# Optimization experiments

Measured on AMD Instinct MI355X. Metric: run time of the kernel, lower is better.

## Reference

```python
import jax, jax.numpy as jnp
import numpy as np

B, S, D, H = 2, 2048, 1024, 16
HD = D // H  # head dim = 64


def setup_inputs() -> dict:
    key = jax.random.key(0)
    ks = jax.random.split(key, 5)
    scale = 0.02
    x = jax.random.normal(ks[0], (B, S, D), dtype=jnp.float32)
    Wqkv = jax.random.normal(ks[1], (D, 3 * D), dtype=jnp.float32) * scale
    bqkv = jnp.zeros((3 * D,), dtype=jnp.float32)
    Wproj = jax.random.normal(ks[2], (D, D), dtype=jnp.float32) * scale
    bproj = jnp.zeros((D,), dtype=jnp.float32)
    return {"x": x, "Wqkv": Wqkv, "bqkv": bqkv, "Wproj": Wproj, "bproj": bproj}


def reference(x, Wqkv, bqkv, Wproj, bproj):
    # fused QKV projection
    qkv = x @ Wqkv + bqkv                      # [B, S, 3D]
    q, k, v = jnp.split(qkv, 3, axis=-1)       # each [B, S, D]
    # split heads -> [B, H, S, HD]
    def heads(t):
        return t.reshape(B, S, H, HD).transpose(0, 2, 1, 3)
    q, k, v = heads(q), heads(k), heads(v)
    # scaled dot-product attention with causal mask (GPT-2 style)
    scores = jnp.einsum('bhqd,bhkd->bhqk', q, k) / jnp.sqrt(jnp.float32(HD))
    causal = jnp.tril(jnp.ones((S, S), dtype=bool))
    scores = jnp.where(causal, scores, jnp.finfo(scores.dtype).min)
    attn = jax.nn.softmax(scores, axis=-1)      # [B, H, S, S]
    out = jnp.einsum('bhqk,bhkd->bhqd', attn, v)  # [B, H, S, HD]
    out = out.transpose(0, 2, 1, 3).reshape(B, S, D)
    return out @ Wproj + bproj
```

## Files before the change

### kernel.cpp

```cpp
#include <hip/hip_runtime.h>
#include <hip/hip_bf16.h>


typedef __attribute__((ext_vector_type(8))) short short8;
typedef __attribute__((ext_vector_type(4))) float float4v;

#define S_LEN 2048
#define NHEAD 16
#define HDIM  64
#define DMODEL 1024

__device__ __forceinline__ unsigned short f2bf(float f) {
    union { float f; unsigned u; } v; v.f = f;
    unsigned r = v.u + 0x7FFF + ((v.u >> 16) & 1);
    return (unsigned short)(r >> 16);
}

__device__ __forceinline__ unsigned fbits_rn(float f) {
    union { float f; unsigned u; } v; v.f = f;
    return v.u + 0x8000u;
}

__device__ __forceinline__ void async16(const void* g, const void* l) {
    __builtin_amdgcn_global_load_lds(
        (const __attribute__((address_space(1))) unsigned int*)g,
        (__attribute__((address_space(3))) unsigned int*)l, 16, 0, 0);
}

__global__ void f32_to_bf16_v4(const float4* __restrict__ in,
                               ushort4* __restrict__ out, int n4) {
    int i = blockIdx.x * blockDim.x + threadIdx.x;
    if (i < n4) {
        float4 v = in[i];
        ushort4 o;
        o.x = f2bf(v.x); o.y = f2bf(v.y); o.z = f2bf(v.z); o.w = f2bf(v.w);
        out[i] = o;
    }
}

__global__ __launch_bounds__(256) void w_transpose_bf16(
    const float* __restrict__ Wqkv, const float* __restrict__ Wproj,
    unsigned short* __restrict__ outQ, unsigned short* __restrict__ outP) {
    __shared__ float t[64][65];
    const float* in; unsigned short* out; int N, bxl;
    if (blockIdx.x < 48) { in = Wqkv;  out = outQ; N = 3072; bxl = blockIdx.x; }
    else                 { in = Wproj; out = outP; N = 1024; bxl = blockIdx.x - 48; }
    const int K = 1024;
    const int kb = blockIdx.y * 64, nb = bxl * 64;
    const int tid = threadIdx.x;
    const int r0 = tid >> 4, c0 = (tid & 15) * 4;
#pragma unroll
    for (int g = 0; g < 4; g++) {
        float4 v = *(const float4*)(in + (size_t)(kb + g * 16 + r0) * N + nb + c0);
        t[g * 16 + r0][c0 + 0] = v.x; t[g * 16 + r0][c0 + 1] = v.y;
        t[g * 16 + r0][c0 + 2] = v.z; t[g * 16 + r0][c0 + 3] = v.w;
    }
    __syncthreads();
#pragma unroll
    for (int g = 0; g < 4; g++) {
        int n = g * 16 + r0;
        ushort4 o;
        o.x = f2bf(t[c0 + 0][n]); o.y = f2bf(t[c0 + 1][n]);
        o.z = f2bf(t[c0 + 2][n]); o.w = f2bf(t[c0 + 3][n]);
        *(ushort4*)(out + (size_t)(nb + n) * K + kb + c0) = o;
    }
}

__global__ __launch_bounds__(256) void v_transpose_sw(
    const unsigned short* __restrict__ V, unsigned short* __restrict__ Vt) {
    __shared__ unsigned short t[64 * 68];
    const int bh = blockIdx.y;
    const int s0 = blockIdx.x * 64;
    const int tid = threadIdx.x;
    const int r = tid >> 2;
    const int c4 = tid & 3;
    const size_t base = (size_t)bh * S_LEN * HDIM;
    union { uint4 v[2]; unsigned short u[16]; } d;
    const unsigned short* src = V + base + (size_t)(s0 + r) * HDIM + c4 * 16;
    d.v[0] = *(const uint4*)(src);
    d.v[1] = *(const uint4*)(src + 8);
#pragma unroll
    for (int j = 0; j < 16; j++) t[(c4 * 16 + j) * 68 + r] = d.u[j];
    __syncthreads();
    const int h4 = r & 15;
    const unsigned short* pl = t + r * 68 + c4 * 16;
    unsigned short* po = Vt + base + (size_t)r * S_LEN + s0
                         + (((c4 * 4) ^ (h4 & 12)) << 2);
    uint2 ug[4];
#pragma unroll
    for (int i = 0; i < 4; i++)
        ug[i ^ (h4 & 3)] = *(const uint2*)(pl + i * 4);
    uint4 w0; w0.x = ug[0].x; w0.y = ug[0].y; w0.z = ug[1].x; w0.w = ug[1].y;
    uint4 w1; w1.x = ug[2].x; w1.y = ug[2].y; w1.z = ug[3].x; w1.w = ug[3].y;
    *(uint4*)(po) = w0;
    *(uint4*)(po + 8) = w1;
}

#define QSCALE 0.18033688f

__global__ __launch_bounds__(256) void gemm_qkv_kernel(
    const unsigned short* __restrict__ A,
    const unsigned short* __restrict__ Bt,
    const float* __restrict__ bias,
    unsigned short* __restrict__ out_q,
    unsigned short* __restrict__ out_k,
    unsigned short* __restrict__ out_v,
    int M, int N, int K)
{
    __shared__ unsigned short smem[128 * 132];
    unsigned short* As = smem;
    unsigned short* Bs = smem + 8192;

    const int tid  = threadIdx.x;
    const int lane = tid & 63;
    const int wave = tid >> 6;
    const int quad = lane >> 4;
    const int l16  = lane & 15;

    const int m0 = blockIdx.y * 128;
    const int n0 = blockIdx.x * 128;
    const int wm = (wave >> 1) * 64;
    const int wn = (wave & 1) * 64;

    float4v acc[4][4];
#pragma unroll
    for (int i = 0; i < 4; i++)
#pragma unroll
        for (int j = 0; j < 4; j++) acc[i][j] = (float4v){0.f, 0.f, 0.f, 0.f};

    const int srow = lane >> 2;
    const int scol = (lane & 3) * 8;

    for (int k0 = 0; k0 < K; k0 += 64) {
        __syncthreads();
#pragma unroll
        for (int kk = 0; kk < 2; kk++)
#pragma unroll
            for (int it = 0; it < 2; it++) {
                const int rg = it * 64 + wave * 16;
                async16(A  + (size_t)(m0 + rg + srow) * K + k0 + kk * 32 + scol,
                        (const char*)(As + kk * 4096) + rg * 64);
                async16(Bt + (size_t)(n0 + rg + srow) * K + k0 + kk * 32 + scol,
                        (const char*)(Bs + kk * 4096) + rg * 64);
            }
        __syncthreads();

#pragma unroll
        for (int kk = 0; kk < 2; kk++) {
            short8 af[4], bf[4];
#pragma unroll
            for (int mt = 0; mt < 4; mt++)
                af[mt] = *(const short8*)(As + kk * 4096
                                          + (wm + mt * 16 + l16) * 32 + quad * 8);
#pragma unroll
            for (int nt = 0; nt < 4; nt++)
                bf[nt] = *(const short8*)(Bs + kk * 4096
                                          + (wn + nt * 16 + l16) * 32 + quad * 8);
#pragma unroll
            for (int mt = 0; mt < 4; mt++)
#pragma unroll
                for (int nt = 0; nt < 4; nt++)
                    acc[mt][nt] = __builtin_amdgcn_mfma_f32_16x16x32_bf16(
                        af[mt], bf[nt], acc[mt][nt], 0, 0, 0);
        }
    }

    __syncthreads();
#pragma unroll
    for (int nt = 0; nt < 4; nt++) {
        const int col = n0 + wn + nt * 16 + l16;
        const float sc = ((col >> 10) == 0) ? QSCALE : 1.0f;
        const float bia = bias[col] * sc;
        const int cold = (wn + nt * 16 + l16) >> 1;
#pragma unroll
        for (int mt = 0; mt < 4; mt++)
#pragma unroll
            for (int r = 0; r < 4; r++) {
                unsigned fb = fbits_rn(acc[mt][nt][r] * sc + bia);
                unsigned fbp = (unsigned)__shfl_xor((int)fb, 1, 64);
                unsigned pd = (l16 & 1)
                    ? __builtin_amdgcn_perm(fb, fbp, 0x07060302)
                    : __builtin_amdgcn_perm(fbp, fb, 0x07060302);
                const int rowl = wm + mt * 16 + quad * 4 + r;
                *((unsigned*)smem + rowl * 66 + cold) = pd;
            }
    }
    __syncthreads();

#pragma unroll
    for (int ps = 0; ps < 8; ps++) {
        const int row = ps * 16 + (tid >> 4);
        const int pc  = tid & 15;
        const int col0 = pc * 8;
        const int haf = col0 >> 6;
        const int cb = n0 + haf * 64;
        const int part = cb >> 10;
        const int h = (cb & 1023) >> 6;
        const int gr = m0 + row;
        const int b = gr >> 11, s = gr & 2047;
        const size_t bhI = (size_t)(b * NHEAD + h);
        const unsigned short* pl = smem + row * 132 + col0;
        uint2 a = *(const uint2*)(pl);
        uint2 bb = *(const uint2*)(pl + 4);
        uint4 w; w.x = a.x; w.y = a.y; w.z = bb.x; w.w = bb.y;
        unsigned short* po;
        if (part == 1) {
            const int plane = (col0 & 63) >> 5;
            po = out_k + ((bhI * 2 + plane) * S_LEN + s) * 32 + (col0 & 31);
        } else {
            unsigned short* dst = (part == 0) ? out_q : out_v;
            po = dst + (bhI * S_LEN + s) * HDIM + (col0 & 63);
        }
        *(uint4*)po = w;
    }
}

__global__ __launch_bounds__(256) void gemm_proj_kernel(
    const unsigned short* __restrict__ A,
    const unsigned short* __restrict__ Bt,
    const float* __restrict__ bias,
    float* __restrict__ out_f,
    int M, int N, int K)
{
    __shared__ unsigned short smem[12288];
    unsigned short* As = smem;
    unsigned short* Bs = smem + 4096;

    const int tid  = threadIdx.x;
    const int lane = tid & 63;
    const int wave = tid >> 6;
    const int quad = lane >> 4;
    const int l16  = lane & 15;

    const int m0 = blockIdx.y * 64;
    const int n0 = blockIdx.x * 128;
    const int wm = (wave >> 1) * 32;
    const int wn = (wave & 1) * 64;

    float4v acc[2][4];
#pragma unroll
    for (int i = 0; i < 2; i++)
#pragma unroll
        for (int j = 0; j < 4; j++) acc[i][j] = (float4v){0.f, 0.f, 0.f, 0.f};

    const int srow = lane >> 2;
    const int scol = (lane & 3) * 8;

    for (int k0 = 0; k0 < K; k0 += 64) {
        __syncthreads();
#pragma unroll
        for (int kk = 0; kk < 2; kk++) {
            async16(A + (size_t)(m0 + wave * 16 + srow) * K + k0 + kk * 32 + scol,
                    (const char*)(As + kk * 2048) + wave * 1024);
#pragma unroll
            for (int it = 0; it < 2; it++) {
                const int rg = it * 64 + wave * 16;
                async16(Bt + (size_t)(n0 + rg + srow) * K + k0 + kk * 32 + scol,
                        (const char*)(Bs + kk * 4096) + rg * 64);
            }
        }
        __syncthreads();

#pragma unroll
        for (int kk = 0; kk < 2; kk++) {
            short8 af[2], bf[4];
#pragma unroll
            for (int mt = 0; mt < 2; mt++)
                af[mt] = *(const short8*)(As + kk * 2048
                                          + (wm + mt * 16 + l16) * 32 + quad * 8);
#pragma unroll
            for (int nt = 0; nt < 4; nt++)
                bf[nt] = *(const short8*)(Bs + kk * 4096
                                          + (wn + nt * 16 + l16) * 32 + quad * 8);
#pragma unroll
            for (int mt = 0; mt < 2; mt++)
#pragma unroll
                for (int nt = 0; nt < 4; nt++)
                    acc[mt][nt] = __builtin_amdgcn_mfma_f32_16x16x32_bf16(
                        af[mt], bf[nt], acc[mt][nt], 0, 0, 0);
        }
    }

#pragma unroll
    for (int nt = 0; nt < 4; nt++) {
        const int col = n0 + wn + nt * 16 + l16;
        const float bia = bias[col];
#pragma unroll
        for (int mt = 0; mt < 2; mt++) {
            const int rowb = m0 + wm + mt * 16 + quad * 4;
#pragma unroll
            for (int r = 0; r < 4; r++)
                out_f[(size_t)(rowb + r) * N + col] = acc[mt][nt][r] + bia;
        }
    }
}

__global__ __launch_bounds__(512) void attn4_kernel(
    const unsigned short* __restrict__ Q,
    const unsigned short* __restrict__ K2,
    const unsigned short* __restrict__ Vt,
    unsigned short* __restrict__ ctx)
{
    __shared__ unsigned short Ks[2][128 * 32];
    __shared__ unsigned short Vs[2][64 * 64];

    const int tid  = threadIdx.x;
    const int lane = tid & 63;
    const int wave = tid >> 6;
    const int quad = lane >> 4;
    const int l16  = lane & 15;

    const int bx = blockIdx.x;
    const int bh = bx & 31;
    const int j  = bx >> 5;
    const int qb = (j < 8) ? (15 - j) : (j - 8);
    const int q0 = qb * 128 + wave * 16;
    const int nch = 2 * qb + 2;

    const size_t baseQ = (size_t)bh * S_LEN * HDIM;
    const size_t baseK = (size_t)bh * 2 * S_LEN * 32;
    const size_t baseV = (size_t)bh * HDIM * S_LEN;

    const int krw = wave * 16 + (lane >> 2);
    const int kcol = (lane & 3) * 8;
    const int vrw = wave * 8 + (lane >> 3);
    const int vcol = (lane & 7) * 8;

    short8 qf[2];
#pragma unroll
    for (int h = 0; h < 2; h++)
        qf[h] = *(const short8*)(Q + baseQ + (size_t)(q0 + l16) * HDIM
                                 + h * 32 + quad * 8);

    float4v o[4];
#pragma unroll
    for (int nt = 0; nt < 4; nt++) o[nt] = (float4v){0.f, 0.f, 0.f, 0.f};
    float lsum = 0.f;

#define ATTN_STAGE(buf, kb0)                                                   \
    do {                                                                       \
        async16(K2 + baseK + ((size_t)(krw >> 6) * S_LEN + (kb0) + (krw & 63)) \
                    * 32 + kcol,                                               \
                (const char*)Ks[buf] + wave * 1024);                           \
        async16(Vt + baseV + (size_t)vrw * S_LEN + (kb0) + vcol,               \
                (const char*)Vs[buf] + wave * 1024);                           \
    } while (0)

    ATTN_STAGE(0, 0);

    for (int c = 0; c < nch; c++) {
        const int buf = c & 1;
        __syncthreads();
        if (c + 1 < nch) ATTN_STAGE(buf ^ 1, (c + 1) * 64);

        const int kb0 = c * 64;
        short8 kf[4][2];
#pragma unroll
        for (int kt = 0; kt < 4; kt++)
#pragma unroll
            for (int h = 0; h < 2; h++)
                kf[kt][h] = *(const short8*)&Ks[buf][(h * 64 + kt * 16 + l16) * 32
                                                     + quad * 8];
        float4v st[4];
#pragma unroll
        for (int kt = 0; kt < 4; kt++) {
            st[kt] = __builtin_amdgcn_mfma_f32_16x16x32_bf16(
                kf[kt][0], qf[0], (float4v){0.f, 0.f, 0.f, 0.f}, 0, 0, 0);
            st[kt] = __builtin_amdgcn_mfma_f32_16x16x32_bf16(
                kf[kt][1], qf[1], st[kt], 0, 0, 0);
        }
        const bool needm = (kb0 + 63 > q0);
        const int qpos = q0 + l16;
        float p[4][4];
#pragma unroll
        for (int kt = 0; kt < 4; kt++)
#pragma unroll
            for (int r = 0; r < 4; r++) {
                float x = st[kt][r];
                if (needm) {
                    int kpos = kb0 + kt * 16 + quad * 4 + r;
                    x = (kpos <= qpos) ? x : -1e30f;
                }
                p[kt][r] = __builtin_amdgcn_exp2f(x);
                lsum += p[kt][r];
            }

        unsigned pk[4][2];
#pragma unroll
        for (int kt = 0; kt < 4; kt++)
#pragma unroll
            for (int jj = 0; jj < 2; jj++)
                pk[kt][jj] = __builtin_amdgcn_perm(
                    fbits_rn(p[kt][2 * jj + 1]), fbits_rn(p[kt][2 * jj]),
                    0x07060302);
        union { unsigned u[4]; short8 s; } pf[2];
#pragma unroll
        for (int kk = 0; kk < 2; kk++)
#pragma unroll
            for (int pp = 0; pp < 4; pp++)
                pf[kk].u[pp] = pk[kk * 2 + (pp >> 1)][pp & 1];

#pragma unroll
        for (int nt = 0; nt < 4; nt++) {
            union { ushort4 h[2]; short8 s; } vf[2];
#pragma unroll
            for (int kt = 0; kt < 4; kt++)
                vf[kt >> 1].h[kt & 1] = *(const ushort4*)&Vs[buf][
                    (nt * 16 + l16) * 64 + (((kt * 4 + quad) ^ l16) << 2)];
            o[nt] = __builtin_amdgcn_mfma_f32_16x16x32_bf16(
                pf[0].s, vf[0].s, o[nt], 0, 0, 0);
            o[nt] = __builtin_amdgcn_mfma_f32_16x16x32_bf16(
                pf[1].s, vf[1].s, o[nt], 0, 0, 0);
        }
    }
#undef ATTN_STAGE

    float l = lsum;
    l += __shfl_xor(l, 16, 64);
    l += __shfl_xor(l, 32, 64);
    const float linv = 1.f / l;
    float lr[4];
#pragma unroll
    for (int r = 0; r < 4; r++) lr[r] = __shfl(linv, quad * 4 + r, 64);

    const int b = bh >> 4, h = bh & 15;
#pragma unroll
    for (int r = 0; r < 4; r++) {
        const int s = q0 + quad * 4 + r;
        const size_t off = ((size_t)(b * S_LEN + s)) * DMODEL + h * HDIM;
#pragma unroll
        for (int nt = 0; nt < 4; nt++)
            ctx[off + nt * 16 + l16] = f2bf(o[nt][r] * lr[r]);
    }
}

extern "C" void kernel_launch(void* const* d_in, const int* in_sizes, int n_in,
                              void* d_out, int out_size, void* d_ws, size_t ws_size,
                              hipStream_t stream) {
    const float* x     = (const float*)d_in[0];
    const float* Wqkv  = (const float*)d_in[1];
    const float* bqkv  = (const float*)d_in[2];
    const float* Wproj = (const float*)d_in[3];
    const float* bproj = (const float*)d_in[4];
    float* out = (float*)d_out;

    const int M  = 2 * S_LEN;
    const int N1 = 3 * DMODEL;
    const int K  = DMODEL;

    unsigned short* x_bf    = (unsigned short*)d_ws;
    unsigned short* wqkv_t  = x_bf   + (size_t)M * K;
    unsigned short* wproj_t = wqkv_t + (size_t)K * N1;
    unsigned short* q_bf    = wproj_t + (size_t)K * DMODEL;
    unsigned short* k_bf    = q_bf   + (size_t)M * DMODEL;
    unsigned short* v_bf    = k_bf   + (size_t)M * DMODEL;
    unsigned short* ctx_bf  = v_bf   + (size_t)M * DMODEL;
    unsigned short* vt_bf   = x_bf;

    {
        int n4 = (M * K) / 4;
        f32_to_bf16_v4<<<n4 / 256, 256, 0, stream>>>((const float4*)x,
                                                     (ushort4*)x_bf, n4);
    }
    {
        dim3 g(64, 16);
        w_transpose_bf16<<<g, 256, 0, stream>>>(Wqkv, Wproj, wqkv_t, wproj_t);
    }

    dim3 g1(N1 / 128, M / 128);
    gemm_qkv_kernel<<<g1, 256, 0, stream>>>(x_bf, wqkv_t, bqkv,
                                            q_bf, k_bf, v_bf, M, N1, K);

    {
        dim3 g(S_LEN / 64, 2 * NHEAD);
        v_transpose_sw<<<g, 256, 0, stream>>>(v_bf, vt_bf);
    }

    attn4_kernel<<<512, 512, 0, stream>>>(q_bf, k_bf, vt_bf, ctx_bf);

    dim3 g3(DMODEL / 128, M / 64);
    gemm_proj_kernel<<<g3, 256, 0, stream>>>(ctx_bf, wproj_t, bproj, out,
                                             M, DMODEL, K);
}
```

Before: 202.5 us.

## Pre-pack K and V into MFMA fragment order, drop LDS staging in attention

The QKV GEMM epilogue now writes K directly in per-lane MFMA fragment order, and the V transpose kernel is replaced by a pack kernel that writes V fragments in the same lane-contiguous order. The attention kernel loads K and V fragments straight from global memory (L2) with 16-byte per-lane loads, removing LDS double-buffering and the per-chunk __syncthreads. Blocks shrink to 256 threads with 64-query tiles (1024 blocks), and masking is applied only on the last chunk. This trades LDS sharing across waves for redundant global/L2 reads by each wave and loses explicit async prefetch overlap.

```diff
diff --git a/kernel.cpp b/kernel.cpp
--- a/kernel.cpp
+++ b/kernel.cpp
@@ -66,34 +66,38 @@
     }
 }
 
-__global__ __launch_bounds__(256) void v_transpose_sw(
-    const unsigned short* __restrict__ V, unsigned short* __restrict__ Vt) {
+__global__ __launch_bounds__(256) void v_pack(
+    const unsigned short* __restrict__ V, unsigned short* __restrict__ Vp) {
     __shared__ unsigned short t[64 * 68];
     const int bh = blockIdx.y;
-    const int s0 = blockIdx.x * 64;
+    const int c0 = blockIdx.x;
+    const int s0 = c0 * 64;
     const int tid = threadIdx.x;
-    const int r = tid >> 2;
-    const int c4 = tid & 3;
+    const int r = tid >> 2, c4 = tid & 3;
     const size_t base = (size_t)bh * S_LEN * HDIM;
     union { uint4 v[2]; unsigned short u[16]; } d;
     const unsigned short* src = V + base + (size_t)(s0 + r) * HDIM + c4 * 16;
     d.v[0] = *(const uint4*)(src);
     d.v[1] = *(const uint4*)(src + 8);
 #pragma unroll
-    for (int j = 0; j < 16; j++) t[(c4 * 16 + j) * 68 + r] = d.u[j];
+    for (int j = 0; j < 16; j++) t[r * 68 + c4 * 16 + j] = d.u[j];
     __syncthreads();
-    const int h4 = r & 15;
-    const unsigned short* pl = t + r * 68 + c4 * 16;
-    unsigned short* po = Vt + base + (size_t)r * S_LEN + s0
-                         + (((c4 * 4) ^ (h4 & 12)) << 2);
-    uint2 ug[4];
-#pragma unroll
-    for (int i = 0; i < 4; i++)
-        ug[i ^ (h4 & 3)] = *(const uint2*)(pl + i * 4);
-    uint4 w0; w0.x = ug[0].x; w0.y = ug[0].y; w0.z = ug[1].x; w0.w = ug[1].y;
-    uint4 w1; w1.x = ug[2].x; w1.y = ug[2].y; w1.z = ug[3].x; w1.w = ug[3].y;
-    *(uint4*)(po) = w0;
-    *(uint4*)(po + 8) = w1;
+    unsigned short* outb = Vp + ((size_t)(bh * 32 + c0)) * 4096;
+#pragma unroll
+    for (int pi = 0; pi < 2; pi++) {
+        const int p = tid * 2 + pi;
+        const int lane = p & 63, kk = (p >> 6) & 1, nt = p >> 7;
+        const int q = lane >> 4, l = lane & 15;
+        union { ushort4 v[2]; unsigned short u[8]; } w;
+#pragma unroll
+        for (int j = 0; j < 8; j++) {
+            const int key = (kk * 2 + (j >> 2)) * 16 + q * 4 + (j & 3);
+            w.u[j] = t[key * 68 + nt * 16 + l];
+        }
+        unsigned short* po = outb + ((nt * 2 + kk) * 64 + lane) * 8;
+        *(ushort4*)(po) = w.v[0];
+        *(ushort4*)(po + 4) = w.v[1];
+    }
 }
 
 #define QSCALE 0.18033688f
@@ -103,7 +107,7 @@
     const unsigned short* __restrict__ Bt,
     const float* __restrict__ bias,
     unsigned short* __restrict__ out_q,
-    unsigned short* __restrict__ out_k,
+    unsigned short* __restrict__ out_kp,
     unsigned short* __restrict__ out_v,
     int M, int N, int K)
 {
@@ -192,21 +196,22 @@
         const int row = ps * 16 + (tid >> 4);
         const int pc  = tid & 15;
         const int col0 = pc * 8;
-        const int haf = col0 >> 6;
-        const int cb = n0 + haf * 64;
+        const int cb = n0 + (col0 >> 6) * 64;
         const int part = cb >> 10;
-        const int h = (cb & 1023) >> 6;
+        const int hh = (cb & 1023) >> 6;
         const int gr = m0 + row;
         const int b = gr >> 11, s = gr & 2047;
-        const size_t bhI = (size_t)(b * NHEAD + h);
+        const size_t bhI = (size_t)(b * NHEAD + hh);
         const unsigned short* pl = smem + row * 132 + col0;
         uint2 a = *(const uint2*)(pl);
         uint2 bb = *(const uint2*)(pl + 4);
         uint4 w; w.x = a.x; w.y = a.y; w.z = bb.x; w.w = bb.y;
         unsigned short* po;
         if (part == 1) {
-            const int plane = (col0 & 63) >> 5;
-            po = out_k + ((bhI * 2 + plane) * S_LEN + s) * 32 + (col0 & 31);
+            const int hd = col0 & 63;
+            const int h = hd >> 5, q = (hd >> 3) & 3;
+            po = out_kp + ((((bhI * 32 + (s >> 6)) * 4 + ((s >> 4) & 3)) * 2 + h)
+                           * 64 + q * 16 + (s & 15)) * 8;
         } else {
             unsigned short* dst = (part == 0) ? out_q : out_v;
             po = dst + (bhI * S_LEN + s) * HDIM + (col0 & 63);
@@ -295,15 +300,12 @@
     }
 }
 
-__global__ __launch_bounds__(512) void attn4_kernel(
+__global__ __launch_bounds__(256) void attn5_kernel(
     const unsigned short* __restrict__ Q,
-    const unsigned short* __restrict__ K2,
-    const unsigned short* __restrict__ Vt,
+    const unsigned short* __restrict__ Kp,
+    const unsigned short* __restrict__ Vp,
     unsigned short* __restrict__ ctx)
 {
-    __shared__ unsigned short Ks[2][128 * 32];
-    __shared__ unsigned short Vs[2][64 * 64];
-
     const int tid  = threadIdx.x;
     const int lane = tid & 63;
     const int wave = tid >> 6;
@@ -312,19 +314,13 @@
 
     const int bx = blockIdx.x;
     const int bh = bx & 31;
-    const int j  = bx >> 5;
-    const int qb = (j < 8) ? (15 - j) : (j - 8);
-    const int q0 = qb * 128 + wave * 16;
-    const int nch = 2 * qb + 2;
+    const int qb = 31 - (bx >> 5);
+    const int q0 = qb * 64 + wave * 16;
+    const int nch = qb + 1;
 
     const size_t baseQ = (size_t)bh * S_LEN * HDIM;
-    const size_t baseK = (size_t)bh * 2 * S_LEN * 32;
-    const size_t baseV = (size_t)bh * HDIM * S_LEN;
-
-    const int krw = wave * 16 + (lane >> 2);
-    const int kcol = (lane & 3) * 8;
-    const int vrw = wave * 8 + (lane >> 3);
-    const int vcol = (lane & 7) * 8;
+    const unsigned short* kb_ = Kp + (size_t)bh * 32 * 4096;
+    const unsigned short* vb_ = Vp + (size_t)bh * 32 * 4096;
 
     short8 qf[2];
 #pragma unroll
@@ -337,30 +333,21 @@
     for (int nt = 0; nt < 4; nt++) o[nt] = (float4v){0.f, 0.f, 0.f, 0.f};
     float lsum = 0.f;
 
-#define ATTN_STAGE(buf, kb0)                                                   \
-    do {                                                                       \
-        async16(K2 + baseK + ((size_t)(krw >> 6) * S_LEN + (kb0) + (krw & 63)) \
-                    * 32 + kcol,                                               \
-                (const char*)Ks[buf] + wave * 1024);                           \
-        async16(Vt + baseV + (size_t)vrw * S_LEN + (kb0) + vcol,               \
-                (const char*)Vs[buf] + wave * 1024);                           \
-    } while (0)
-
-    ATTN_STAGE(0, 0);
-
     for (int c = 0; c < nch; c++) {
-        const int buf = c & 1;
-        __syncthreads();
-        if (c + 1 < nch) ATTN_STAGE(buf ^ 1, (c + 1) * 64);
-
-        const int kb0 = c * 64;
-        short8 kf[4][2];
+        const unsigned short* kc = kb_ + (size_t)c * 4096;
+        const unsigned short* vc = vb_ + (size_t)c * 4096;
+        short8 kf[4][2], vf[4][2];
 #pragma unroll
         for (int kt = 0; kt < 4; kt++)
 #pragma unroll
             for (int h = 0; h < 2; h++)
-                kf[kt][h] = *(const short8*)&Ks[buf][(h * 64 + kt * 16 + l16) * 32
-                                                     + quad * 8];
+                kf[kt][h] = *(const short8*)(kc + ((kt * 2 + h) * 64 + lane) * 8);
+#pragma unroll
+        for (int nt = 0; nt < 4; nt++)
+#pragma unroll
+            for (int kk = 0; kk < 2; kk++)
+                vf[nt][kk] = *(const short8*)(vc + ((nt * 2 + kk) * 64 + lane) * 8);
+
         float4v st[4];
 #pragma unroll
         for (int kt = 0; kt < 4; kt++) {
@@ -369,7 +356,8 @@
             st[kt] = __builtin_amdgcn_mfma_f32_16x16x32_bf16(
                 kf[kt][1], qf[1], st[kt], 0, 0, 0);
         }
-        const bool needm = (kb0 + 63 > q0);
+        const bool lastc = (c == nch - 1);
+        const int kb0 = c * 64;
         const int qpos = q0 + l16;
         float p[4][4];
 #pragma unroll
@@ -377,7 +365,7 @@
 #pragma unroll
             for (int r = 0; r < 4; r++) {
                 float x = st[kt][r];
-                if (needm) {
+                if (lastc) {
                     int kpos = kb0 + kt * 16 + quad * 4 + r;
                     x = (kpos <= qpos) ? x : -1e30f;
                 }
@@ -389,9 +377,9 @@
 #pragma unroll
         for (int kt = 0; kt < 4; kt++)
 #pragma unroll
-            for (int jj = 0; jj < 2; jj++)
-                pk[kt][jj] = __builtin_amdgcn_perm(
-                    fbits_rn(p[kt][2 * jj + 1]), fbits_rn(p[kt][2 * jj]),
+            for (int j = 0; j < 2; j++)
+                pk[kt][j] = __builtin_amdgcn_perm(
+                    fbits_rn(p[kt][2 * j + 1]), fbits_rn(p[kt][2 * j]),
                     0x07060302);
         union { unsigned u[4]; short8 s; } pf[2];
 #pragma unroll
@@ -402,18 +390,12 @@
 
 #pragma unroll
         for (int nt = 0; nt < 4; nt++) {
-            union { ushort4 h[2]; short8 s; } vf[2];
-#pragma unroll
-            for (int kt = 0; kt < 4; kt++)
-                vf[kt >> 1].h[kt & 1] = *(const ushort4*)&Vs[buf][
-                    (nt * 16 + l16) * 64 + (((kt * 4 + quad) ^ l16) << 2)];
             o[nt] = __builtin_amdgcn_mfma_f32_16x16x32_bf16(
-                pf[0].s, vf[0].s, o[nt], 0, 0, 0);
+                pf[0].s, vf[nt][0], o[nt], 0, 0, 0);
             o[nt] = __builtin_amdgcn_mfma_f32_16x16x32_bf16(
-                pf[1].s, vf[1].s, o[nt], 0, 0, 0);
-        }
-    }
-#undef ATTN_STAGE
+                pf[1].s, vf[nt][1], o[nt], 0, 0, 0);
+        }
+    }
 
     float l = lsum;
     l += __shfl_xor(l, 16, 64);
@@ -452,10 +434,10 @@
     unsigned short* wqkv_t  = x_bf   + (size_t)M * K;
     unsigned short* wproj_t = wqkv_t + (size_t)K * N1;
     unsigned short* q_bf    = wproj_t + (size_t)K * DMODEL;
-    unsigned short* k_bf    = q_bf   + (size_t)M * DMODEL;
-    unsigned short* v_bf    = k_bf   + (size_t)M * DMODEL;
+    unsigned short* kp_bf   = q_bf   + (size_t)M * DMODEL;
+    unsigned short* v_bf    = kp_bf  + (size_t)M * DMODEL;
     unsigned short* ctx_bf  = v_bf   + (size_t)M * DMODEL;
-    unsigned short* vt_bf   = x_bf;
+    unsigned short* vp_bf   = x_bf;
 
     {
         int n4 = (M * K) / 4;
@@ -469,14 +451,14 @@
 
     dim3 g1(N1 / 128, M / 128);
     gemm_qkv_kernel<<<g1, 256, 0, stream>>>(x_bf, wqkv_t, bqkv,
-                                            q_bf, k_bf, v_bf, M, N1, K);
+                                            q_bf, kp_bf, v_bf, M, N1, K);
 
     {
         dim3 g(S_LEN / 64, 2 * NHEAD);
-        v_transpose_sw<<<g, 256, 0, stream>>>(v_bf, vt_bf);
-    }
-
-    attn4_kernel<<<512, 512, 0, stream>>>(q_bf, k_bf, vt_bf, ctx_bf);
+        v_pack<<<g, 256, 0, stream>>>(v_bf, vp_bf);
+    }
+
+    attn5_kernel<<<1024, 256, 0, stream>>>(q_bf, kp_bf, vp_bf, ctx_bf);
 
     dim3 g3(DMODEL / 128, M / 64);
     gemm_proj_kernel<<<g3, 256, 0, stream>>>(ctx_bf, wproj_t, bproj, out,
```

Result: faster. 188.1 us (-7.1%).
